# Performance work log

Hardware: AMD Instinct MI355X
Metric: run time of the kernel (lower is better)

Reference implementation:

```python
import jax, jax.numpy as jnp
import numpy as np

N_NODES = 100000
N_EDGES = 1600000
IN_C, HID_C, OUT_C = 128, 256, 128


def setup_inputs() -> dict:
    key = jax.random.key(0)
    ks = jax.random.split(key, 8)
    x = jax.random.normal(ks[0], (N_NODES, IN_C), dtype=jnp.float32)
    edge_row = jax.random.randint(ks[1], (N_EDGES,), 0, N_NODES, dtype=jnp.int32)
    edge_col = jax.random.randint(ks[2], (N_EDGES,), 0, N_NODES, dtype=jnp.int32)
    # normalized adjacency values (e.g. D^-1/2 A D^-1/2 entries), positive
    edge_vals = jax.random.uniform(ks[3], (N_EDGES,), dtype=jnp.float32) * 0.1
    # torch Linear weights: y = x @ W.T + b (xavier scale)
    W1 = jax.random.normal(ks[4], (HID_C, IN_C), dtype=jnp.float32) * (2.0 / (IN_C + HID_C)) ** 0.5
    b1 = jnp.zeros((HID_C,), dtype=jnp.float32)
    W2 = jax.random.normal(ks[5], (HID_C, HID_C), dtype=jnp.float32) * (1.0 / HID_C) ** 0.5
    b2 = jnp.zeros((HID_C,), dtype=jnp.float32)
    W3 = jax.random.normal(ks[6], (OUT_C, HID_C), dtype=jnp.float32) * (2.0 / (HID_C + OUT_C)) ** 0.5
    b3 = jnp.zeros((OUT_C,), dtype=jnp.float32)
    return {"x": x, "edge_row": edge_row, "edge_col": edge_col, "edge_vals": edge_vals,
            "W1": W1, "b1": b1, "W2": W2, "b2": b2, "W3": W3, "b3": b3}


def reference(x, edge_row, edge_col, edge_vals, W1, b1, W2, b2, W3, b3):
    n = x.shape[0]

    def spmm(h):
        # out[i] = sum over edges e with row[e]==i of vals[e] * h[col[e]]
        msgs = h[edge_col] * edge_vals[:, None]          # [E, C]
        return jax.ops.segment_sum(msgs, edge_row, num_segments=n)

    h = jax.nn.relu(spmm(x) @ W1.T + b1)                 # GCNConv 1 + relu
    h = jax.nn.relu(spmm(h) @ W2.T + b2)                 # GCNConv 2 + relu
    h = spmm(h) @ W3.T + b3                              # GCNConv 3 (no act)
    # F.normalize: L2 along dim=1 with eps clamp 1e-12
    norm = jnp.linalg.norm(h, axis=1, keepdims=True)
    return h / jnp.maximum(norm, 1e-12)
```

## Files before the change

kernel.cpp:

```cpp
#include <hip/hip_runtime.h>
#include <hip/hip_bf16.h>

#define N_NODES 100000
#define N_EDGES 1600000
#define IN_C 128
#define HID_C 256
#define OUT_C 128

typedef __attribute__((ext_vector_type(8))) short bf16x8;
typedef __attribute__((ext_vector_type(4))) float f32x4;
typedef __attribute__((ext_vector_type(2))) float f32x2;

static __device__ __forceinline__ short f2bf(float f) {
    union { float f; unsigned u; } x{f};
    unsigned r = (x.u + 0x7fffu + ((x.u >> 16) & 1u)) >> 16;
    return (short)r;
}
static __device__ __forceinline__ f32x2 bfpair(unsigned d) {
    union { unsigned u; float f; } lo, hi;
    lo.u = d << 16;
    hi.u = d & 0xffff0000u;
    return f32x2{lo.f, hi.f};
}

__global__ void hist_rank(const int* __restrict__ rows, int* __restrict__ deg,
                          int* __restrict__ rank, int E)
{
    int e = blockIdx.x * blockDim.x + threadIdx.x;
    if (e < E) rank[e] = atomicAdd(&deg[rows[e]], 1);
}

#define SCAN_BLOCK 256
#define SCAN_ELEMS 1024

__global__ __launch_bounds__(SCAN_BLOCK) void scan1(const int* __restrict__ deg,
                                                    int* __restrict__ excl,
                                                    int* __restrict__ bsum, int N)
{
    __shared__ int sh[SCAN_BLOCK];
    int t = threadIdx.x;
    int base = blockIdx.x * SCAN_ELEMS + t * 4;
    int v[4];
    #pragma unroll
    for (int i = 0; i < 4; ++i) {
        int idx = base + i;
        v[i] = (idx < N) ? deg[idx] : 0;
    }
    int s = v[0] + v[1] + v[2] + v[3];
    sh[t] = s;
    __syncthreads();
    for (int d = 1; d < SCAN_BLOCK; d <<= 1) {
        int add = (t >= d) ? sh[t - d] : 0;
        __syncthreads();
        sh[t] += add;
        __syncthreads();
    }
    int p = sh[t] - s;
    #pragma unroll
    for (int i = 0; i < 4; ++i) {
        int idx = base + i;
        if (idx < N) excl[idx] = p;
        p += v[i];
    }
    if (t == SCAN_BLOCK - 1) bsum[blockIdx.x] = sh[t];
}

__global__ void scan3(int* __restrict__ row_start, const int* __restrict__ bsum,
                      int NB, int N, int E)
{
    __shared__ int pref[128];
    int t = threadIdx.x;
    if (t < 128) pref[t] = (t < NB) ? bsum[t] : 0;
    __syncthreads();
    for (int d = 1; d < 128; d <<= 1) {
        int add = (t < 128 && t >= d) ? pref[t - d] : 0;
        __syncthreads();
        if (t < 128) pref[t] += add;
        __syncthreads();
    }
    int i = blockIdx.x * blockDim.x + t;
    if (i < N) {
        int b = i >> 10;
        row_start[i] += (b == 0) ? 0 : pref[b - 1];
    } else if (i == N) {
        row_start[N] = E;
    }
}

__global__ void scatter_cast(const int* __restrict__ rows, const int* __restrict__ cols,
                             const float* __restrict__ vals, const int* __restrict__ row_start,
                             const int* __restrict__ rank, int2* __restrict__ epk, int E,
                             const float* __restrict__ s0, short* __restrict__ d0, int n0,
                             const float* __restrict__ s1, short* __restrict__ d1, int n1,
                             const float* __restrict__ s2, short* __restrict__ d2, int n2,
                             const float* __restrict__ s3, short* __restrict__ d3, int n3)
{
    int idx = blockIdx.x * blockDim.x + threadIdx.x;
    if (idx < E) {
        int pos = row_start[rows[idx]] + rank[idx];
        epk[pos] = int2{cols[idx], __float_as_int(vals[idx])};
    } else {
        int i = (idx - E) * 4;
        int castN = n0 + n1 + n2 + n3;
        if (i >= castN) return;
        const float* s; short* d;
        if (i < n0) { s = s0; d = d0; }
        else if ((i -= n0) < n1) { s = s1; d = d1; }
        else if ((i -= n1) < n2) { s = s2; d = d2; }
        else { i -= n2; s = s3; d = d3; }
        float4 v = *(const float4*)(s + i);
        *(short4*)(d + i) = short4{f2bf(v.x), f2bf(v.y), f2bf(v.z), f2bf(v.w)};
    }
}

template<int B, int ND>
static __device__ __forceinline__ void spmm_batch(
    const unsigned* __restrict__ Hb, const int2* __restrict__ epk,
    int j, int loff, f32x2* acc)
{
    int2 e[B];
    #pragma unroll
    for (int b = 0; b < B; ++b) e[b] = epk[j + b];
    uint2 g[B];
    #pragma unroll
    for (int b = 0; b < B; ++b) {
        const unsigned* p = Hb + (size_t)e[b].x * (64 * ND) + loff;
        if constexpr (ND == 2) g[b] = *(const uint2*)p;
        else                   g[b].x = *p;
    }
    #pragma unroll
    for (int b = 0; b < B; ++b) {
        float v = __int_as_float(e[b].y);
        acc[0] += v * bfpair(g[b].x);
        if constexpr (ND == 2) acc[1] += v * bfpair(g[b].y);
    }
}

template<int C, int MODE>
__global__ __launch_bounds__(256) void spmm_gather(
    const short* __restrict__ H, const int* __restrict__ row_start,
    const int2* __restrict__ epk, void* __restrict__ outv,
    const float* __restrict__ bias, int N)
{
    constexpr int PL = C / 64;
    constexpr int ND = PL / 2;
    int wid = threadIdx.x >> 6;
    int lane = threadIdx.x & 63;
    int row = blockIdx.x * 4 + wid;
    if (row >= N) return;
    int j = row_start[row];
    int end = row_start[row + 1];
    const unsigned* Hb = (const unsigned*)H;
    const int loff = lane * ND;

    f32x2 acc[ND];
    #pragma unroll
    for (int d = 0; d < ND; ++d) acc[d] = f32x2{0.f, 0.f};

    for (; j + 8 <= end; j += 8) spmm_batch<8, ND>(Hb, epk, j, loff, acc);
    if (j + 4 <= end) { spmm_batch<4, ND>(Hb, epk, j, loff, acc); j += 4; }
    if (j + 2 <= end) { spmm_batch<2, ND>(Hb, epk, j, loff, acc); j += 2; }
    if (j < end)      { spmm_batch<1, ND>(Hb, epk, j, loff, acc); }

    if constexpr (MODE == 0) {
        unsigned od[ND];
        #pragma unroll
        for (int d = 0; d < ND; ++d)
            od[d] = (unsigned)(unsigned short)f2bf(acc[d].x)
                  | ((unsigned)(unsigned short)f2bf(acc[d].y) << 16);
        unsigned* orow = (unsigned*)outv + (size_t)row * (64 * ND) + loff;
        if constexpr (ND == 2) *(uint2*)orow = uint2{od[0], od[1]};
        else                   *orow = od[0];
    } else {
        int ch = lane * 2;
        float o0 = acc[0].x + bias[ch];
        float o1 = acc[0].y + bias[ch + 1];
        float ss = o0 * o0 + o1 * o1;
        #pragma unroll
        for (int d = 1; d < 64; d <<= 1)
            ss += __shfl_xor(ss, d);
        float s = 1.0f / fmaxf(sqrtf(ss), 1e-12f);
        *(float2*)((float*)outv + (size_t)row * C + ch) = float2{o0 * s, o1 * s};
    }
}

template<int K, int M, bool RELU, bool BIAS>
__global__ __launch_bounds__(256) void gemm_bf16(
    const short* __restrict__ A, const short* __restrict__ W,
    const float* __restrict__ bias, short* __restrict__ Y, int N)
{
    constexpr int MBLK = M / 64;
    constexpr int BK = 32;
    constexpr int PAD = 8;
    __shared__ short As[128][BK + PAD];
    __shared__ short Ws[64][BK + PAD];

    const int id = blockIdx.x;
    const int bx = (id / (8 * MBLK)) * 8 + (id & 7);
    const int by = (id >> 3) & (MBLK - 1);

    const int tid = threadIdx.x;
    const int wid = tid >> 6;
    const int lane = tid & 63;
    const int wm = wid & 1;
    const int wn = wid >> 1;
    const int l15 = lane & 15;
    const int quad = lane >> 4;
    const int bn = bx * 128;
    const int bm = by * 64;

    f32x4 acc[4][2] = {};

    for (int k0 = 0; k0 < K; k0 += BK) {
        #pragma unroll
        for (int c = 0; c < 2; ++c) {
            int chunk = tid + c * 256;
            int row = chunk >> 2;
            int koff = (chunk & 3) * 8;
            int gr = bn + row;
            ulonglong2 v = {0ull, 0ull};
            if (gr < N) v = *(const ulonglong2*)(A + (size_t)gr * K + k0 + koff);
            *(ulonglong2*)&As[row][koff] = v;
        }
        {
            int row = tid >> 2;
            int koff = (tid & 3) * 8;
            ulonglong2 v = *(const ulonglong2*)(W + (size_t)(bm + row) * K + k0 + koff);
            *(ulonglong2*)&Ws[row][koff] = v;
        }
        __syncthreads();

        bf16x8 aF[4], bF[2];
        #pragma unroll
        for (int mt = 0; mt < 4; ++mt)
            aF[mt] = *(const bf16x8*)&As[wm * 64 + mt * 16 + l15][quad * 8];
        #pragma unroll
        for (int nt = 0; nt < 2; ++nt)
            bF[nt] = *(const bf16x8*)&Ws[wn * 32 + nt * 16 + l15][quad * 8];

        #pragma unroll
        for (int mt = 0; mt < 4; ++mt)
            #pragma unroll
            for (int nt = 0; nt < 2; ++nt)
                acc[mt][nt] = __builtin_amdgcn_mfma_f32_16x16x32_bf16(
                    aF[mt], bF[nt], acc[mt][nt], 0, 0, 0);
        __syncthreads();
    }

    #pragma unroll
    for (int nt = 0; nt < 2; ++nt) {
        int col = bm + wn * 32 + nt * 16 + l15;
        float bv = BIAS ? bias[col] : 0.f;
        #pragma unroll
        for (int mt = 0; mt < 4; ++mt) {
            int row0 = bn + wm * 64 + mt * 16 + quad * 4;
            #pragma unroll
            for (int r = 0; r < 4; ++r) {
                int row = row0 + r;
                if (row < N) {
                    float v = acc[mt][nt][r] + bv;
                    if (RELU) v = fmaxf(v, 0.f);
                    Y[(size_t)row * M + col] = f2bf(v);
                }
            }
        }
    }
}

extern "C" void kernel_launch(void* const* d_in, const int* in_sizes, int n_in,
                              void* d_out, int out_size, void* d_ws, size_t ws_size,
                              hipStream_t stream) {
    const float* x        = (const float*)d_in[0];
    const int*   edge_row = (const int*)d_in[1];
    const int*   edge_col = (const int*)d_in[2];
    const float* edge_val = (const float*)d_in[3];
    const float* W1       = (const float*)d_in[4];
    const float* b1       = (const float*)d_in[5];
    const float* W2       = (const float*)d_in[6];
    const float* b2       = (const float*)d_in[7];
    const float* W3       = (const float*)d_in[8];
    const float* b3       = (const float*)d_in[9];
    float* out = (float*)d_out;

    const int N = N_NODES, E = N_EDGES;
    const int NB = (N + SCAN_ELEMS - 1) / SCAN_ELEMS;

    short* xbf = (short*)d_ws;
    short* Hbf = xbf + (size_t)N * IN_C;
    short* Gbf = Hbf + (size_t)N * HID_C;
    short* W1b = Gbf + (size_t)N * HID_C;
    short* W2b = W1b + HID_C * IN_C;
    short* W3b = W2b + HID_C * HID_C;
    int* deg = (int*)(((uintptr_t)(W3b + OUT_C * HID_C) + 15) & ~(uintptr_t)15);
    int* row_start = deg + N;
    int* rank      = row_start + (N + 1);
    int* bsum      = rank + E;
    int2* epk      = (int2*)(((uintptr_t)(bsum + 128) + 15) & ~(uintptr_t)15);

    hipMemsetAsync(deg, 0, N * sizeof(int), stream);
    hist_rank<<<(E + 255) / 256, 256, 0, stream>>>(edge_row, deg, rank, E);
    scan1<<<NB, SCAN_BLOCK, 0, stream>>>(deg, row_start, bsum, N);
    scan3<<<(N + 256) / 256, 256, 0, stream>>>(row_start, bsum, NB, N, E);
    {
        int n0 = N * IN_C, n1 = HID_C * IN_C, n2 = HID_C * HID_C, n3 = OUT_C * HID_C;
        int total = E + (n0 + n1 + n2 + n3) / 4;
        scatter_cast<<<(total + 255) / 256, 256, 0, stream>>>(
            edge_row, edge_col, edge_val, row_start, rank, epk, E,
            x, xbf, n0, W1, W1b, n1, W2, W2b, n2, W3, W3b, n3);
    }

    const int spmm_grid = (N + 3) / 4;
    const int GXP = ((N + 127) / 128 + 7) & ~7;

    spmm_gather<IN_C, 0><<<spmm_grid, 256, 0, stream>>>(
        xbf, row_start, epk, Hbf, nullptr, N);
    gemm_bf16<IN_C, HID_C, true, true><<<GXP * (HID_C / 64), 256, 0, stream>>>(
        Hbf, W1b, b1, Gbf, N);

    spmm_gather<HID_C, 0><<<spmm_grid, 256, 0, stream>>>(
        Gbf, row_start, epk, Hbf, nullptr, N);
    gemm_bf16<HID_C, HID_C, true, true><<<GXP * (HID_C / 64), 256, 0, stream>>>(
        Hbf, W2b, b2, Gbf, N);

    gemm_bf16<HID_C, OUT_C, false, false><<<GXP * (OUT_C / 64), 256, 0, stream>>>(
        Gbf, W3b, nullptr, Hbf, N);
    spmm_gather<OUT_C, 2><<<spmm_grid, 256, 0, stream>>>(
        Hbf, row_start, epk, out, b3, N);
}
```

Before: 566.5 us.

## Fuse SpMM gather with following dense GEMM per 64-row tile

Replaces separate spmm_gather and gemm_bf16 launches with a fused kernel: each block aggregates 64 rows into LDS, then multiplies by the weight matrix read directly from global memory. The second layer also chains the W3 GEMM in-block, so layer 2 and the layer-3 transform are one kernel. This removes the intermediate HBM write and read of the aggregated features and two launches. In exchange, weights are fetched per block without LDS staging, and the gather phase runs serially per wave over 16 rows, which may lower gather parallelism.

Measured after the change: 633.1 us. +11.8%, slower.

```diff
diff --git a/kernel.cpp b/kernel.cpp
--- a/kernel.cpp
+++ b/kernel.cpp
@@ -184,83 +184,148 @@
     }
 }
 
-template<int K, int M, bool RELU, bool BIAS>
-__global__ __launch_bounds__(256) void gemm_bf16(
-    const short* __restrict__ A, const short* __restrict__ W,
-    const float* __restrict__ bias, short* __restrict__ Y, int N)
-{
-    constexpr int MBLK = M / 64;
-    constexpr int BK = 32;
-    constexpr int PAD = 8;
-    __shared__ short As[128][BK + PAD];
-    __shared__ short Ws[64][BK + PAD];
-
-    const int id = blockIdx.x;
-    const int bx = (id / (8 * MBLK)) * 8 + (id & 7);
-    const int by = (id >> 3) & (MBLK - 1);
+template<int CIN, int COUT, bool FUSE3, int C3>
+__global__ __launch_bounds__(256, 4) void spmm_gemm(
+    const short* __restrict__ H, const int* __restrict__ row_start,
+    const int2* __restrict__ epk,
+    const short* __restrict__ W, const float* __restrict__ bias,
+    const short* __restrict__ W3,
+    short* __restrict__ Y, short* __restrict__ Y3, int N)
+{
+    static_assert(!FUSE3 || CIN == COUT, "phase-C restages into the same LDS tile");
+    constexpr int ND = CIN / 128;
+    constexpr int LDW = CIN + 8;
+    __shared__ short As[64][LDW];
 
     const int tid = threadIdx.x;
     const int wid = tid >> 6;
     const int lane = tid & 63;
+    const int rb = blockIdx.x * 64;
+
+    {
+        const unsigned* Hb = (const unsigned*)H;
+        const int loff = lane * ND;
+        for (int rr = 0; rr < 16; ++rr) {
+            const int lr = wid * 16 + rr;
+            const int row = rb + lr;
+            f32x2 acc[ND];
+            #pragma unroll
+            for (int d = 0; d < ND; ++d) acc[d] = f32x2{0.f, 0.f};
+            if (row < N) {
+                int j = row_start[row];
+                const int end = row_start[row + 1];
+                for (; j + 8 <= end; j += 8) spmm_batch<8, ND>(Hb, epk, j, loff, acc);
+                if (j + 4 <= end) { spmm_batch<4, ND>(Hb, epk, j, loff, acc); j += 4; }
+                if (j + 2 <= end) { spmm_batch<2, ND>(Hb, epk, j, loff, acc); j += 2; }
+                if (j < end)      spmm_batch<1, ND>(Hb, epk, j, loff, acc);
+            }
+            if constexpr (ND == 2) {
+                unsigned o0 = (unsigned)(unsigned short)f2bf(acc[0].x)
+                            | ((unsigned)(unsigned short)f2bf(acc[0].y) << 16);
+                unsigned o1 = (unsigned)(unsigned short)f2bf(acc[1].x)
+                            | ((unsigned)(unsigned short)f2bf(acc[1].y) << 16);
+                *(uint2*)&As[lr][4 * lane] = uint2{o0, o1};
+            } else {
+                unsigned o0 = (unsigned)(unsigned short)f2bf(acc[0].x)
+                            | ((unsigned)(unsigned short)f2bf(acc[0].y) << 16);
+                *(unsigned*)&As[lr][2 * lane] = o0;
+            }
+        }
+    }
+    __syncthreads();
+
     const int wm = wid & 1;
     const int wn = wid >> 1;
     const int l15 = lane & 15;
     const int quad = lane >> 4;
-    const int bn = bx * 128;
-    const int bm = by * 64;
-
-    f32x4 acc[4][2] = {};
-
-    for (int k0 = 0; k0 < K; k0 += BK) {
-        #pragma unroll
-        for (int c = 0; c < 2; ++c) {
-            int chunk = tid + c * 256;
-            int row = chunk >> 2;
-            int koff = (chunk & 3) * 8;
-            int gr = bn + row;
-            ulonglong2 v = {0ull, 0ull};
-            if (gr < N) v = *(const ulonglong2*)(A + (size_t)gr * K + k0 + koff);
-            *(ulonglong2*)&As[row][koff] = v;
-        }
-        {
-            int row = tid >> 2;
-            int koff = (tid & 3) * 8;
-            ulonglong2 v = *(const ulonglong2*)(W + (size_t)(bm + row) * K + k0 + koff);
-            *(ulonglong2*)&Ws[row][koff] = v;
-        }
-        __syncthreads();
-
-        bf16x8 aF[4], bF[2];
-        #pragma unroll
-        for (int mt = 0; mt < 4; ++mt)
-            aF[mt] = *(const bf16x8*)&As[wm * 64 + mt * 16 + l15][quad * 8];
-        #pragma unroll
-        for (int nt = 0; nt < 2; ++nt)
-            bF[nt] = *(const bf16x8*)&Ws[wn * 32 + nt * 16 + l15][quad * 8];
-
-        #pragma unroll
-        for (int mt = 0; mt < 4; ++mt)
-            #pragma unroll
-            for (int nt = 0; nt < 2; ++nt)
-                acc[mt][nt] = __builtin_amdgcn_mfma_f32_16x16x32_bf16(
-                    aF[mt], bF[nt], acc[mt][nt], 0, 0, 0);
-        __syncthreads();
-    }
-
-    #pragma unroll
-    for (int nt = 0; nt < 2; ++nt) {
-        int col = bm + wn * 32 + nt * 16 + l15;
-        float bv = BIAS ? bias[col] : 0.f;
-        #pragma unroll
-        for (int mt = 0; mt < 4; ++mt) {
-            int row0 = bn + wm * 64 + mt * 16 + quad * 4;
-            #pragma unroll
-            for (int r = 0; r < 4; ++r) {
-                int row = row0 + r;
-                if (row < N) {
-                    float v = acc[mt][nt][r] + bv;
-                    if (RELU) v = fmaxf(v, 0.f);
-                    Y[(size_t)row * M + col] = f2bf(v);
+    constexpr int NT = COUT / 32;
+    f32x4 acc[2][NT] = {};
+
+    for (int k0 = 0; k0 < CIN; k0 += 32) {
+        bf16x8 aF[2];
+        #pragma unroll
+        for (int mt = 0; mt < 2; ++mt)
+            aF[mt] = *(const bf16x8*)&As[wm * 32 + mt * 16 + l15][k0 + quad * 8];
+        #pragma unroll
+        for (int nc = 0; nc < NT; nc += 4) {
+            bf16x8 bF[4];
+            #pragma unroll
+            for (int i = 0; i < 4; ++i) {
+                const int col = wn * (COUT / 2) + (nc + i) * 16 + l15;
+                bF[i] = *(const bf16x8*)&W[(size_t)col * CIN + k0 + quad * 8];
+            }
+            #pragma unroll
+            for (int mt = 0; mt < 2; ++mt)
+                #pragma unroll
+                for (int i = 0; i < 4; ++i)
+                    acc[mt][nc + i] = __builtin_amdgcn_mfma_f32_16x16x32_bf16(
+                        aF[mt], bF[i], acc[mt][nc + i], 0, 0, 0);
+        }
+    }
+
+    if constexpr (!FUSE3) {
+        #pragma unroll
+        for (int nt = 0; nt < NT; ++nt) {
+            const int col = wn * (COUT / 2) + nt * 16 + l15;
+            const float bv = bias[col];
+            #pragma unroll
+            for (int mt = 0; mt < 2; ++mt) {
+                const int row0 = rb + wm * 32 + mt * 16 + quad * 4;
+                #pragma unroll
+                for (int r = 0; r < 4; ++r) {
+                    const int row = row0 + r;
+                    if (row < N)
+                        Y[(size_t)row * COUT + col] = f2bf(fmaxf(acc[mt][nt][r] + bv, 0.f));
+                }
+            }
+        }
+    } else {
+        __syncthreads();
+        #pragma unroll
+        for (int nt = 0; nt < NT; ++nt) {
+            const int col = wn * (COUT / 2) + nt * 16 + l15;
+            const float bv = bias[col];
+            #pragma unroll
+            for (int mt = 0; mt < 2; ++mt) {
+                const int lr0 = wm * 32 + mt * 16 + quad * 4;
+                #pragma unroll
+                for (int r = 0; r < 4; ++r)
+                    As[lr0 + r][col] = f2bf(fmaxf(acc[mt][nt][r] + bv, 0.f));
+            }
+        }
+        __syncthreads();
+
+        constexpr int NT3 = C3 / 32;
+        f32x4 acc3[2][NT3] = {};
+        for (int k0 = 0; k0 < COUT; k0 += 32) {
+            bf16x8 aF[2];
+            #pragma unroll
+            for (int mt = 0; mt < 2; ++mt)
+                aF[mt] = *(const bf16x8*)&As[wm * 32 + mt * 16 + l15][k0 + quad * 8];
+            bf16x8 bF[NT3];
+            #pragma unroll
+            for (int nt = 0; nt < NT3; ++nt) {
+                const int col = wn * (C3 / 2) + nt * 16 + l15;
+                bF[nt] = *(const bf16x8*)&W3[(size_t)col * COUT + k0 + quad * 8];
+            }
+            #pragma unroll
+            for (int mt = 0; mt < 2; ++mt)
+                #pragma unroll
+                for (int nt = 0; nt < NT3; ++nt)
+                    acc3[mt][nt] = __builtin_amdgcn_mfma_f32_16x16x32_bf16(
+                        aF[mt], bF[nt], acc3[mt][nt], 0, 0, 0);
+        }
+        #pragma unroll
+        for (int nt = 0; nt < NT3; ++nt) {
+            const int col = wn * (C3 / 2) + nt * 16 + l15;
+            #pragma unroll
+            for (int mt = 0; mt < 2; ++mt) {
+                const int row0 = rb + wm * 32 + mt * 16 + quad * 4;
+                #pragma unroll
+                for (int r = 0; r < 4; ++r) {
+                    const int row = row0 + r;
+                    if (row < N)
+                        Y3[(size_t)row * C3 + col] = f2bf(acc3[mt][nt][r]);
                 }
             }
         }
@@ -286,8 +351,7 @@
     const int NB = (N + SCAN_ELEMS - 1) / SCAN_ELEMS;
 
     short* xbf = (short*)d_ws;
-    short* Hbf = xbf + (size_t)N * IN_C;
-    short* Gbf = Hbf + (size_t)N * HID_C;
+    short* Gbf = xbf + (size_t)N * IN_C;
     short* W1b = Gbf + (size_t)N * HID_C;
     short* W2b = W1b + HID_C * IN_C;
     short* W3b = W2b + HID_C * HID_C;
@@ -309,21 +373,14 @@
             x, xbf, n0, W1, W1b, n1, W2, W2b, n2, W3, W3b, n3);
     }
 
-    const int spmm_grid = (N + 3) / 4;
-    const int GXP = ((N + 127) / 128 + 7) & ~7;
-
-    spmm_gather<IN_C, 0><<<spmm_grid, 256, 0, stream>>>(
-        xbf, row_start, epk, Hbf, nullptr, N);
-    gemm_bf16<IN_C, HID_C, true, true><<<GXP * (HID_C / 64), 256, 0, stream>>>(
-        Hbf, W1b, b1, Gbf, N);
-
-    spmm_gather<HID_C, 0><<<spmm_grid, 256, 0, stream>>>(
-        Gbf, row_start, epk, Hbf, nullptr, N);
-    gemm_bf16<HID_C, HID_C, true, true><<<GXP * (HID_C / 64), 256, 0, stream>>>(
-        Hbf, W2b, b2, Gbf, N);
-
-    gemm_bf16<HID_C, OUT_C, false, false><<<GXP * (OUT_C / 64), 256, 0, stream>>>(
-        Gbf, W3b, nullptr, Hbf, N);
-    spmm_gather<OUT_C, 2><<<spmm_grid, 256, 0, stream>>>(
-        Hbf, row_start, epk, out, b3, N);
-}
+    const int fgrid = (N + 63) / 64;
+
+    spmm_gemm<IN_C, HID_C, false, 0><<<fgrid, 256, 0, stream>>>(
+        xbf, row_start, epk, W1b, b1, nullptr, Gbf, nullptr, N);
+
+    spmm_gemm<HID_C, HID_C, true, OUT_C><<<fgrid, 256, 0, stream>>>(
+        Gbf, row_start, epk, W2b, b2, W3b, nullptr, xbf, N);
+
+    spmm_gather<OUT_C, 2><<<(N + 3) / 4, 256, 0, stream>>>(
+        xbf, row_start, epk, out, b3, N);
+}
```

## Fuse layer-2 and layer-3 GEMMs; split SpMM wave into half-wave edge pairs

Applied to the files above, without the earlier changes.

Adds a fused gemm23 kernel that computes relu(A·W2ᵀ+b2) into LDS and immediately multiplies by W3ᵀ, so the 256-wide intermediate is never written to or read back from global memory. The SpMM gather kernel now has each half-wave handle alternate edges with wider 8- or 16-byte loads per lane. The two halves are then combined with a cross-half shuffle, and the launch bounds ask for higher occupancy. In the fused kernel, W2 and W3 fragments are read straight from global memory rather than staged in LDS, which may add L2 traffic.

Measured after the change: 772.1 us. 1.36x slower.

```diff
diff --git a/kernel.cpp b/kernel.cpp
--- a/kernel.cpp
+++ b/kernel.cpp
@@ -113,74 +113,114 @@
     }
 }
 
-template<int B, int ND>
-static __device__ __forceinline__ void spmm_batch(
+template<int B, int NU>
+static __device__ __forceinline__ void pair_batch(
     const unsigned* __restrict__ Hb, const int2* __restrict__ epk,
-    int j, int loff, f32x2* acc)
-{
-    int2 e[B];
-    #pragma unroll
-    for (int b = 0; b < B; ++b) e[b] = epk[j + b];
-    uint2 g[B];
+    int j, bool hi, int loff, f32x2* acc)
+{
+    int2 ea[B], eb[B];
+    #pragma unroll
+    for (int b = 0; b < B; ++b) { ea[b] = epk[j + 2 * b]; eb[b] = epk[j + 2 * b + 1]; }
+    unsigned g[B][NU];
     #pragma unroll
     for (int b = 0; b < B; ++b) {
-        const unsigned* p = Hb + (size_t)e[b].x * (64 * ND) + loff;
-        if constexpr (ND == 2) g[b] = *(const uint2*)p;
-        else                   g[b].x = *p;
+        const int col = hi ? eb[b].x : ea[b].x;
+        const unsigned* p = Hb + (size_t)col * (32 * NU) + loff;
+        if constexpr (NU == 4) {
+            uint4 t = *(const uint4*)p;
+            g[b][0] = t.x; g[b][1] = t.y; g[b][2] = t.z; g[b][3] = t.w;
+        } else {
+            uint2 t = *(const uint2*)p;
+            g[b][0] = t.x; g[b][1] = t.y;
+        }
     }
     #pragma unroll
     for (int b = 0; b < B; ++b) {
-        float v = __int_as_float(e[b].y);
-        acc[0] += v * bfpair(g[b].x);
-        if constexpr (ND == 2) acc[1] += v * bfpair(g[b].y);
-    }
+        const float v = __int_as_float(hi ? eb[b].y : ea[b].y);
+        #pragma unroll
+        for (int u = 0; u < NU; ++u) acc[u] += v * bfpair(g[b][u]);
+    }
+}
+
+template<int NU>
+static __device__ __forceinline__ void edge_tail(
+    const unsigned* __restrict__ Hb, const int2* __restrict__ epk,
+    int j, bool hi, int loff, f32x2* acc)
+{
+    int2 e = epk[j];
+    const unsigned* p = Hb + (size_t)e.x * (32 * NU) + loff;
+    unsigned g[NU];
+    if constexpr (NU == 4) {
+        uint4 t = *(const uint4*)p;
+        g[0] = t.x; g[1] = t.y; g[2] = t.z; g[3] = t.w;
+    } else {
+        uint2 t = *(const uint2*)p;
+        g[0] = t.x; g[1] = t.y;
+    }
+    const float v = hi ? 0.f : __int_as_float(e.y);
+    #pragma unroll
+    for (int u = 0; u < NU; ++u) acc[u] += v * bfpair(g[u]);
 }
 
 template<int C, int MODE>
-__global__ __launch_bounds__(256) void spmm_gather(
+__global__ __launch_bounds__(256, 8) void spmm_gather(
     const short* __restrict__ H, const int* __restrict__ row_start,
     const int2* __restrict__ epk, void* __restrict__ outv,
     const float* __restrict__ bias, int N)
 {
-    constexpr int PL = C / 64;
-    constexpr int ND = PL / 2;
-    int wid = threadIdx.x >> 6;
-    int lane = threadIdx.x & 63;
-    int row = blockIdx.x * 4 + wid;
+    constexpr int NU = C / 64;
+    const int wid = threadIdx.x >> 6;
+    const int lane = threadIdx.x & 63;
+    const bool hi = lane >= 32;
+    const int l31 = lane & 31;
+    const int loff = l31 * NU;
+    const int row = blockIdx.x * 4 + wid;
     if (row >= N) return;
     int j = row_start[row];
-    int end = row_start[row + 1];
+    const int end = row_start[row + 1];
     const unsigned* Hb = (const unsigned*)H;
-    const int loff = lane * ND;
-
-    f32x2 acc[ND];
-    #pragma unroll
-    for (int d = 0; d < ND; ++d) acc[d] = f32x2{0.f, 0.f};
-
-    for (; j + 8 <= end; j += 8) spmm_batch<8, ND>(Hb, epk, j, loff, acc);
-    if (j + 4 <= end) { spmm_batch<4, ND>(Hb, epk, j, loff, acc); j += 4; }
-    if (j + 2 <= end) { spmm_batch<2, ND>(Hb, epk, j, loff, acc); j += 2; }
-    if (j < end)      { spmm_batch<1, ND>(Hb, epk, j, loff, acc); }
+
+    f32x2 acc[NU];
+    #pragma unroll
+    for (int u = 0; u < NU; ++u) acc[u] = f32x2{0.f, 0.f};
+
+    for (; j + 16 <= end; j += 16) pair_batch<8, NU>(Hb, epk, j, hi, loff, acc);
+    if (j + 8 <= end) { pair_batch<4, NU>(Hb, epk, j, hi, loff, acc); j += 8; }
+    if (j + 4 <= end) { pair_batch<2, NU>(Hb, epk, j, hi, loff, acc); j += 4; }
+    if (j + 2 <= end) { pair_batch<1, NU>(Hb, epk, j, hi, loff, acc); j += 2; }
+    if (j < end)      edge_tail<NU>(Hb, epk, j, hi, loff, acc);
+
+    #pragma unroll
+    for (int u = 0; u < NU; ++u) {
+        acc[u].x += __shfl_xor(acc[u].x, 32);
+        acc[u].y += __shfl_xor(acc[u].y, 32);
+    }
 
     if constexpr (MODE == 0) {
-        unsigned od[ND];
-        #pragma unroll
-        for (int d = 0; d < ND; ++d)
-            od[d] = (unsigned)(unsigned short)f2bf(acc[d].x)
-                  | ((unsigned)(unsigned short)f2bf(acc[d].y) << 16);
-        unsigned* orow = (unsigned*)outv + (size_t)row * (64 * ND) + loff;
-        if constexpr (ND == 2) *(uint2*)orow = uint2{od[0], od[1]};
-        else                   *orow = od[0];
+        if (lane < 32) {
+            unsigned od[NU];
+            #pragma unroll
+            for (int u = 0; u < NU; ++u)
+                od[u] = (unsigned)(unsigned short)f2bf(acc[u].x)
+                      | ((unsigned)(unsigned short)f2bf(acc[u].y) << 16);
+            unsigned* orow = (unsigned*)outv + (size_t)row * (32 * NU) + loff;
+            if constexpr (NU == 4) *(uint4*)orow = uint4{od[0], od[1], od[2], od[3]};
+            else                   *(uint2*)orow = uint2{od[0], od[1]};
+        }
     } else {
-        int ch = lane * 2;
-        float o0 = acc[0].x + bias[ch];
-        float o1 = acc[0].y + bias[ch + 1];
-        float ss = o0 * o0 + o1 * o1;
-        #pragma unroll
-        for (int d = 1; d < 64; d <<= 1)
+        const int c0 = l31 * 4;
+        float o0 = acc[0].x + bias[c0];
+        float o1 = acc[0].y + bias[c0 + 1];
+        float o2 = acc[1].x + bias[c0 + 2];
+        float o3 = acc[1].y + bias[c0 + 3];
+        float ss = o0 * o0 + o1 * o1 + o2 * o2 + o3 * o3;
+        #pragma unroll
+        for (int d = 1; d < 32; d <<= 1)
             ss += __shfl_xor(ss, d);
         float s = 1.0f / fmaxf(sqrtf(ss), 1e-12f);
-        *(float2*)((float*)outv + (size_t)row * C + ch) = float2{o0 * s, o1 * s};
+        if (lane < 32)
+            *(float4*)((float*)outv + (size_t)row * C + c0) =
+                float4{o0 * s, o1 * s, o2 * s, o3 * s};
     }
 }
 
@@ -262,6 +302,113 @@
                     if (RELU) v = fmaxf(v, 0.f);
                     Y[(size_t)row * M + col] = f2bf(v);
                 }
+            }
+        }
+    }
+}
+
+template<int CIN, int COUT, int C3>
+__global__ __launch_bounds__(256, 4) void gemm23(
+    const short* __restrict__ A,
+    const short* __restrict__ W2, const float* __restrict__ bias2,
+    const short* __restrict__ W3,
+    short* __restrict__ Y3, int N)
+{
+    constexpr int LDW = CIN + 8;
+    __shared__ short As[64][LDW];
+
+    const int tid = threadIdx.x;
+    const int wid = tid >> 6;
+    const int lane = tid & 63;
+    const int rb = blockIdx.x * 64;
+
+    #pragma unroll
+    for (int c = 0; c < (64 * CIN) / (8 * 256); ++c) {
+        int chunk = tid + c * 256;
+        int row = chunk / (CIN / 8);
+        int koff = (chunk % (CIN / 8)) * 8;
+        int gr = rb + row;
+        ulonglong2 v = {0ull, 0ull};
+        if (gr < N) v = *(const ulonglong2*)(A + (size_t)gr * CIN + koff);
+        *(ulonglong2*)&As[row][koff] = v;
+    }
+    __syncthreads();
+
+    const int wm = wid & 1;
+    const int wn = wid >> 1;
+    const int l15 = lane & 15;
+    const int quad = lane >> 4;
+
+    constexpr int NT = COUT / 32;
+    f32x4 acc[2][NT] = {};
+    for (int k0 = 0; k0 < CIN; k0 += 32) {
+        bf16x8 aF[2];
+        #pragma unroll
+        for (int mt = 0; mt < 2; ++mt)
+            aF[mt] = *(const bf16x8*)&As[wm * 32 + mt * 16 + l15][k0 + quad * 8];
+        #pragma unroll
+        for (int nc = 0; nc < NT; nc += 4) {
+            bf16x8 bF[4];
+            #pragma unroll
+            for (int i = 0; i < 4; ++i) {
+                const int col = wn * (COUT / 2) + (nc + i) * 16 + l15;
+                bF[i] = *(const bf16x8*)&W2[(size_t)col * CIN + k0 + quad * 8];
+            }
+            #pragma unroll
+            for (int mt = 0; mt < 2; ++mt)
+                #pragma unroll
+                for (int i = 0; i < 4; ++i)
+                    acc[mt][nc + i] = __builtin_amdgcn_mfma_f32_16x16x32_bf16(
+                        aF[mt], bF[i], acc[mt][nc + i], 0, 0, 0);
+        }
+    }
+
+    __syncthreads();
+    #pragma unroll
+    for (int nt = 0; nt < NT; ++nt) {
+        const int col = wn * (COUT / 2) + nt * 16 + l15;
+        const float bv = bias2[col];
+        #pragma unroll
+        for (int mt = 0; mt < 2; ++mt) {
+            const int lr0 = wm * 32 + mt * 16 + quad * 4;
+            #pragma unroll
+            for (int r = 0; r < 4; ++r)
+                As[lr0 + r][col] = f2bf(fmaxf(acc[mt][nt][r] + bv, 0.f));
+        }
+    }
+    __syncthreads();
+
+    constexpr int NT3 = C3 / 32;
+    f32x4 acc3[2][NT3] = {};
+    for (int k0 = 0; k0 < COUT; k0 += 32) {
+        bf16x8 aF[2];
+        #pragma unroll
+        for (int mt = 0; mt < 2; ++mt)
+            aF[mt] = *(const bf16x8*)&As[wm * 32 + mt * 16 + l15][k0 + quad * 8];
+        bf16x8 bF[NT3];
+        #pragma unroll
+        for (int nt = 0; nt < NT3; ++nt) {
+            const int col = wn * (C3 / 2) + nt * 16 + l15;
+            bF[nt] = *(const bf16x8*)&W3[(size_t)col * COUT + k0 + quad * 8];
+        }
+        #pragma unroll
+        for (int mt = 0; mt < 2; ++mt)
+            #pragma unroll
+            for (int nt = 0; nt < NT3; ++nt)
+                acc3[mt][nt] = __builtin_amdgcn_mfma_f32_16x16x32_bf16(
+                    aF[mt], bF[nt], acc3[mt][nt], 0, 0, 0);
+    }
+    #pragma unroll
+    for (int nt = 0; nt < NT3; ++nt) {
+        const int col = wn * (C3 / 2) + nt * 16 + l15;
+        #pragma unroll
+        for (int mt = 0; mt < 2; ++mt) {
+            const int row0 = rb + wm * 32 + mt * 16 + quad * 4;
+            #pragma unroll
+            for (int r = 0; r < 4; ++r) {
+                const int row = row0 + r;
+                if (row < N)
+                    Y3[(size_t)row * C3 + col] = f2bf(acc3[mt][nt][r]);
             }
         }
     }
@@ -311,6 +458,7 @@
 
     const int spmm_grid = (N + 3) / 4;
     const int GXP = ((N + 127) / 128 + 7) & ~7;
+    const int fgrid = (N + 63) / 64;
 
     spmm_gather<IN_C, 0><<<spmm_grid, 256, 0, stream>>>(
         xbf, row_start, epk, Hbf, nullptr, N);
@@ -319,11 +467,10 @@
 
     spmm_gather<HID_C, 0><<<spmm_grid, 256, 0, stream>>>(
         Gbf, row_start, epk, Hbf, nullptr, N);
-    gemm_bf16<HID_C, HID_C, true, true><<<GXP * (HID_C / 64), 256, 0, stream>>>(
-        Hbf, W2b, b2, Gbf, N);
-
-    gemm_bf16<HID_C, OUT_C, false, false><<<GXP * (OUT_C / 64), 256, 0, stream>>>(
-        Gbf, W3b, nullptr, Hbf, N);
+
+    gemm23<HID_C, HID_C, OUT_C><<<fgrid, 256, 0, stream>>>(
+        Hbf, W2b, b2, W3b, xbf, N);
+
     spmm_gather<OUT_C, 2><<<spmm_grid, 256, 0, stream>>>(
-        Hbf, row_start, epk, out, b3, N);
-}
+        xbf, row_start, epk, out, b3, N);
+}
```

## Split wavefront across multiple edges per row with 16-byte gathers in SpMM

Applied to the files above, without the earlier changes.

Restructures the SpMM gather kernels so each 64-lane wavefront processes 4 edges (128-channel rows) or 2 edges (256-channel rows) at once. Each lane loads 16 bytes per gather instead of 4 or 8, and partial sums are combined with cross-lane shuffles at the end. The aim is more memory-level parallelism and wider loads per edge. In exchange it adds shuffle reductions, handles remainder edges with masked loads, and leaves some lanes idle during stores.

After: 562.9 us. No clear change (-0.6%).

```diff
diff --git a/kernel.cpp b/kernel.cpp
--- a/kernel.cpp
+++ b/kernel.cpp
@@ -113,74 +113,164 @@
     }
 }
 
-template<int B, int ND>
-static __device__ __forceinline__ void spmm_batch(
+template<int B>
+static __device__ __forceinline__ void quad_batch(
     const unsigned* __restrict__ Hb, const int2* __restrict__ epk,
-    int j, int loff, f32x2* acc)
+    int j, int sel, int loff, f32x2* acc)
 {
     int2 e[B];
     #pragma unroll
-    for (int b = 0; b < B; ++b) e[b] = epk[j + b];
-    uint2 g[B];
+    for (int b = 0; b < B; ++b) e[b] = epk[j + 4 * b + sel];
+    uint4 g[B];
+    #pragma unroll
+    for (int b = 0; b < B; ++b)
+        g[b] = *(const uint4*)(Hb + (size_t)e[b].x * 64 + loff);
     #pragma unroll
     for (int b = 0; b < B; ++b) {
-        const unsigned* p = Hb + (size_t)e[b].x * (64 * ND) + loff;
-        if constexpr (ND == 2) g[b] = *(const uint2*)p;
-        else                   g[b].x = *p;
-    }
-    #pragma unroll
-    for (int b = 0; b < B; ++b) {
-        float v = __int_as_float(e[b].y);
+        const float v = __int_as_float(e[b].y);
         acc[0] += v * bfpair(g[b].x);
-        if constexpr (ND == 2) acc[1] += v * bfpair(g[b].y);
-    }
-}
-
-template<int C, int MODE>
-__global__ __launch_bounds__(256) void spmm_gather(
+        acc[1] += v * bfpair(g[b].y);
+        acc[2] += v * bfpair(g[b].z);
+        acc[3] += v * bfpair(g[b].w);
+    }
+}
+
+template<int MODE>
+__global__ __launch_bounds__(256) void spmm_gather_q(
     const short* __restrict__ H, const int* __restrict__ row_start,
     const int2* __restrict__ epk, void* __restrict__ outv,
     const float* __restrict__ bias, int N)
 {
-    constexpr int PL = C / 64;
-    constexpr int ND = PL / 2;
-    int wid = threadIdx.x >> 6;
-    int lane = threadIdx.x & 63;
-    int row = blockIdx.x * 4 + wid;
+    const int wid = threadIdx.x >> 6;
+    const int lane = threadIdx.x & 63;
+    const int sel = lane >> 4;
+    const int l15 = lane & 15;
+    const int loff = l15 * 4;
+    const int row = blockIdx.x * 4 + wid;
     if (row >= N) return;
     int j = row_start[row];
-    int end = row_start[row + 1];
+    const int end = row_start[row + 1];
     const unsigned* Hb = (const unsigned*)H;
-    const int loff = lane * ND;
-
-    f32x2 acc[ND];
-    #pragma unroll
-    for (int d = 0; d < ND; ++d) acc[d] = f32x2{0.f, 0.f};
-
-    for (; j + 8 <= end; j += 8) spmm_batch<8, ND>(Hb, epk, j, loff, acc);
-    if (j + 4 <= end) { spmm_batch<4, ND>(Hb, epk, j, loff, acc); j += 4; }
-    if (j + 2 <= end) { spmm_batch<2, ND>(Hb, epk, j, loff, acc); j += 2; }
-    if (j < end)      { spmm_batch<1, ND>(Hb, epk, j, loff, acc); }
+
+    f32x2 acc[4] = {};
+
+    for (; j + 16 <= end; j += 16) quad_batch<4>(Hb, epk, j, sel, loff, acc);
+    for (; j + 4 <= end; j += 4)   quad_batch<1>(Hb, epk, j, sel, loff, acc);
+    if (j < end) {
+        const int rem = end - j;
+        int2 e = epk[j + (sel < rem ? sel : rem - 1)];
+        uint4 g = *(const uint4*)(Hb + (size_t)e.x * 64 + loff);
+        const float v = (sel < rem) ? __int_as_float(e.y) : 0.f;
+        acc[0] += v * bfpair(g.x);
+        acc[1] += v * bfpair(g.y);
+        acc[2] += v * bfpair(g.z);
+        acc[3] += v * bfpair(g.w);
+    }
+
+    #pragma unroll
+    for (int u = 0; u < 4; ++u) {
+        acc[u].x += __shfl_xor(acc[u].x, 16);
+        acc[u].y += __shfl_xor(acc[u].y, 16);
+        acc[u].x += __shfl_xor(acc[u].x, 32);
+        acc[u].y += __shfl_xor(acc[u].y, 32);
+    }
 
     if constexpr (MODE == 0) {
-        unsigned od[ND];
-        #pragma unroll
-        for (int d = 0; d < ND; ++d)
-            od[d] = (unsigned)(unsigned short)f2bf(acc[d].x)
-                  | ((unsigned)(unsigned short)f2bf(acc[d].y) << 16);
-        unsigned* orow = (unsigned*)outv + (size_t)row * (64 * ND) + loff;
-        if constexpr (ND == 2) *(uint2*)orow = uint2{od[0], od[1]};
-        else                   *orow = od[0];
+        if (lane < 16) {
+            unsigned od[4];
+            #pragma unroll
+            for (int u = 0; u < 4; ++u)
+                od[u] = (unsigned)(unsigned short)f2bf(acc[u].x)
+                      | ((unsigned)(unsigned short)f2bf(acc[u].y) << 16);
+            *(uint4*)((unsigned*)outv + (size_t)row * 64 + loff) =
+                uint4{od[0], od[1], od[2], od[3]};
+        }
     } else {
-        int ch = lane * 2;
-        float o0 = acc[0].x + bias[ch];
-        float o1 = acc[0].y + bias[ch + 1];
-        float ss = o0 * o0 + o1 * o1;
-        #pragma unroll
-        for (int d = 1; d < 64; d <<= 1)
+        const int c0 = l15 * 8;
+        float4 b0 = *(const float4*)(bias + c0);
+        float4 b1 = *(const float4*)(bias + c0 + 4);
+        float o0 = acc[0].x + b0.x, o1 = acc[0].y + b0.y;
+        float o2 = acc[1].x + b0.z, o3 = acc[1].y + b0.w;
+        float o4 = acc[2].x + b1.x, o5 = acc[2].y + b1.y;
+        float o6 = acc[3].x + b1.z, o7 = acc[3].y + b1.w;
+        float ss = o0*o0 + o1*o1 + o2*o2 + o3*o3 + o4*o4 + o5*o5 + o6*o6 + o7*o7;
+        #pragma unroll
+        for (int d = 1; d < 16; d <<= 1)
             ss += __shfl_xor(ss, d);
         float s = 1.0f / fmaxf(sqrtf(ss), 1e-12f);
-        *(float2*)((float*)outv + (size_t)row * C + ch) = float2{o0 * s, o1 * s};
+        if (lane < 16) {
+            float* orow = (float*)outv + (size_t)row * 128 + c0;
+            *(float4*)orow       = float4{o0 * s, o1 * s, o2 * s, o3 * s};
+            *(float4*)(orow + 4) = float4{o4 * s, o5 * s, o6 * s, o7 * s};
+        }
+    }
+}
+
+template<int B>
+static __device__ __forceinline__ void pair256_batch(
+    const unsigned* __restrict__ Hb, const int2* __restrict__ epk,
+    int j, int sel, int loff, f32x2* acc)
+{
+    int2 e[B];
+    #pragma unroll
+    for (int b = 0; b < B; ++b) e[b] = epk[j + 2 * b + sel];
+    uint4 g[B];
+    #pragma unroll
+    for (int b = 0; b < B; ++b)
+        g[b] = *(const uint4*)(Hb + (size_t)e[b].x * 128 + loff);
+    #pragma unroll
+    for (int b = 0; b < B; ++b) {
+        const float v = __int_as_float(e[b].y);
+        acc[0] += v * bfpair(g[b].x);
+        acc[1] += v * bfpair(g[b].y);
+        acc[2] += v * bfpair(g[b].z);
+        acc[3] += v * bfpair(g[b].w);
+    }
+}
+
+__global__ __launch_bounds__(256) void spmm_gather_p256(
+    const short* __restrict__ H, const int* __restrict__ row_start,
+    const int2* __restrict__ epk, void* __restrict__ outv, int N)
+{
+    const int wid = threadIdx.x >> 6;
+    const int lane = threadIdx.x & 63;
+    const int sel = lane >> 5;
+    const int l31 = lane & 31;
+    const int loff = l31 * 4;
+    const int row = blockIdx.x * 4 + wid;
+    if (row >= N) return;
+    int j = row_start[row];
+    const int end = row_start[row + 1];
+    const unsigned* Hb = (const unsigned*)H;
+
+    f32x2 acc[4] = {};
+
+    for (; j + 8 <= end; j += 8) pair256_batch<4>(Hb, epk, j, sel, loff, acc);
+    for (; j + 2 <= end; j += 2) pair256_batch<1>(Hb, epk, j, sel, loff, acc);
+    if (j < end) {
+        int2 e = epk[j];
+        uint4 g = *(const uint4*)(Hb + (size_t)e.x * 128 + loff);
+        const float v = sel ? 0.f : __int_as_float(e.y);
+        acc[0] += v * bfpair(g.x);
+        acc[1] += v * bfpair(g.y);
+        acc[2] += v * bfpair(g.z);
+        acc[3] += v * bfpair(g.w);
+    }
+
+    #pragma unroll
+    for (int u = 0; u < 4; ++u) {
+        acc[u].x += __shfl_xor(acc[u].x, 32);
+        acc[u].y += __shfl_xor(acc[u].y, 32);
+    }
+
+    if (lane < 32) {
+        unsigned od[4];
+        #pragma unroll
+        for (int u = 0; u < 4; ++u)
+            od[u] = (unsigned)(unsigned short)f2bf(acc[u].x)
+                  | ((unsigned)(unsigned short)f2bf(acc[u].y) << 16);
+        *(uint4*)((unsigned*)outv + (size_t)row * 128 + loff) =
+            uint4{od[0], od[1], od[2], od[3]};
     }
 }
 
@@ -312,18 +402,18 @@
     const int spmm_grid = (N + 3) / 4;
     const int GXP = ((N + 127) / 128 + 7) & ~7;
 
-    spmm_gather<IN_C, 0><<<spmm_grid, 256, 0, stream>>>(
+    spmm_gather_q<0><<<spmm_grid, 256, 0, stream>>>(
         xbf, row_start, epk, Hbf, nullptr, N);
     gemm_bf16<IN_C, HID_C, true, true><<<GXP * (HID_C / 64), 256, 0, stream>>>(
         Hbf, W1b, b1, Gbf, N);
 
-    spmm_gather<HID_C, 0><<<spmm_grid, 256, 0, stream>>>(
-        Gbf, row_start, epk, Hbf, nullptr, N);
+    spmm_gather_p256<<<spmm_grid, 256, 0, stream>>>(
+        Gbf, row_start, epk, Hbf, N);
     gemm_bf16<HID_C, HID_C, true, true><<<GXP * (HID_C / 64), 256, 0, stream>>>(
         Hbf, W2b, b2, Gbf, N);
 
     gemm_bf16<HID_C, OUT_C, false, false><<<GXP * (OUT_C / 64), 256, 0, stream>>>(
         Gbf, W3b, nullptr, Hbf, N);
-    spmm_gather<OUT_C, 2><<<spmm_grid, 256, 0, stream>>>(
+    spmm_gather_q<2><<<spmm_grid, 256, 0, stream>>>(
         Hbf, row_start, epk, out, b3, N);
 }
```
